# Performance work log

Measured on AMD Instinct MI355X. Metric: run time of the kernel, lower is better.

## Reference

```python
import jax, jax.numpy as jnp
import numpy as np

B, L = 2, 2048
D_MODEL, D_INNER, D_STATE, DT_RANK, D_CONV, DEPTH = 1024, 2048, 16, 64, 4, 2
EPS = 1e-5


def setup_inputs() -> dict:
    key = jax.random.key(0)
    ks = jax.random.split(key, 8)
    rn = lambda k, s, scale=0.02: jax.random.normal(k, s, jnp.float32) * scale
    return {
        "x": jax.random.normal(ks[0], (B, L, D_MODEL), jnp.float32),
        "x_size": L,  # truthiness flag only; unused in the math
        "norm_w": jnp.ones((DEPTH, D_MODEL), jnp.float32),
        "norm_b": jnp.zeros((DEPTH, D_MODEL), jnp.float32),
        "in_proj_w": rn(ks[1], (DEPTH, 2 * D_INNER, D_MODEL)),
        "conv_w": rn(ks[2], (DEPTH, D_INNER, 1, D_CONV), 0.1),
        "conv_b": jnp.zeros((DEPTH, D_INNER), jnp.float32),
        "x_proj_w": rn(ks[3], (DEPTH, DT_RANK + 2 * D_STATE, D_INNER)),
        "dt_proj_w": rn(ks[4], (DEPTH, D_INNER, DT_RANK), 0.1),
        "dt_proj_b": jnp.full((DEPTH, D_INNER), -4.0, jnp.float32),  # softplus -> small dt
        "A_log": jnp.broadcast_to(
            jnp.log(jnp.arange(1, D_STATE + 1, dtype=jnp.float32)), (DEPTH, D_INNER, D_STATE)
        ) + jnp.zeros((DEPTH, D_INNER, D_STATE), jnp.float32),
        "D": jnp.ones((DEPTH, D_INNER), jnp.float32),
        "out_proj_w": rn(ks[5], (DEPTH, D_MODEL, D_INNER)),
    }


def _layernorm(x, w, b):
    mu = x.mean(-1, keepdims=True)
    var = ((x - mu) ** 2).mean(-1, keepdims=True)
    return (x - mu) * jax.lax.rsqrt(var + EPS) * w + b


def _selective_scan(u, dt, A, Bm, Cm, Dp):
    # u, dt: (B, L, di); A: (di, n); Bm, Cm: (B, L, n); Dp: (di,)
    def step(h, inp):
        u_t, dt_t, B_t, C_t = inp  # (B,di), (B,di), (B,n), (B,n)
        dA = jnp.exp(dt_t[..., None] * A)                       # (B, di, n)
        h = dA * h + (dt_t * u_t)[..., None] * B_t[:, None, :]  # (B, di, n)
        y = jnp.einsum('bdn,bn->bd', h, C_t)
        return h, y

    h0 = jnp.zeros((u.shape[0], A.shape[0], A.shape[1]), u.dtype)
    xs = (u.swapaxes(0, 1), dt.swapaxes(0, 1), Bm.swapaxes(0, 1), Cm.swapaxes(0, 1))
    _, ys = jax.lax.scan(step, h0, xs)  # ys: (L, B, di)
    return ys.swapaxes(0, 1) + u * Dp


def _mamba(x, in_proj_w, conv_w, conv_b, x_proj_w, dt_proj_w, dt_proj_b, A_log, Dp, out_proj_w):
    xz = jnp.einsum('bld,ed->ble', x, in_proj_w)  # (B, L, 2*di)
    u, z = jnp.split(xz, 2, axis=-1)
    # causal depthwise conv1d, kernel D_CONV
    uc = jax.lax.conv_general_dilated(
        u.swapaxes(1, 2), conv_w, (1,), [(D_CONV - 1, 0)],
        feature_group_count=D_INNER, dimension_numbers=('NCH', 'OIH', 'NCH'))
    u = jax.nn.silu(uc.swapaxes(1, 2) + conv_b)
    x_dbl = jnp.einsum('bld,ed->ble', u, x_proj_w)
    dt_r, Bm, Cm = jnp.split(x_dbl, [DT_RANK, DT_RANK + D_STATE], axis=-1)
    dt = jax.nn.softplus(jnp.einsum('blr,dr->bld', dt_r, dt_proj_w) + dt_proj_b)
    A = -jnp.exp(A_log)
    y = _selective_scan(u, dt, A, Bm, Cm, Dp)
    y = y * jax.nn.silu(z)
    return jnp.einsum('bld,ed->ble', y, out_proj_w)


def reference(x, x_size, norm_w, norm_b, in_proj_w, conv_w, conv_b, x_proj_w,
              dt_proj_w, dt_proj_b, A_log, D, out_proj_w):
    # BasicLayer passes x_size as `residual` (non-None), so each Block reduces to
    # x <- Mamba(LN(x)); the returned residual is discarded by x = blk(...)[0].
    h = x
    for i in range(DEPTH):
        hn = _layernorm(h, norm_w[i], norm_b[i])
        h = _mamba(hn, in_proj_w[i], conv_w[i], conv_b[i], x_proj_w[i],
                   dt_proj_w[i], dt_proj_b[i], A_log[i], D[i], out_proj_w[i])
    return h
```

## Files before the change

### kernel.cpp

```cpp
#include <hip/hip_runtime.h>
#include <hip/hip_bf16.h>
#include <math.h>

#define BQ 2
#define LQ 2048
#define D_MODEL 1024
#define D_INNER 2048
#define D_STATE 16
#define DT_RANK 64
#define D_CONV 4
#define DEPTH 2
#define NCHUNK 64
#define CHUNK 32
#define XSPLITK 8
#define XKC (D_INNER / XSPLITK)

typedef __attribute__((ext_vector_type(8))) short short8v;
typedef __attribute__((ext_vector_type(4))) float f32x4;

__device__ __forceinline__ short f2bf(float f) {
    union { float f; unsigned u; } v; v.f = f;
    unsigned r = v.u + 0x7fffu + ((v.u >> 16) & 1u);
    return (short)(r >> 16);
}

__device__ __forceinline__ float bf2f(unsigned short s) {
    union { unsigned u; float f; } v; v.u = ((unsigned)s) << 16;
    return v.f;
}

__device__ __forceinline__ void async16(void* lds, const void* gp) {
    __builtin_amdgcn_global_load_lds(
        (const __attribute__((address_space(1))) void*)gp,
        (__attribute__((address_space(3))) void*)lds, 16, 0, 0);
}

__global__ __launch_bounds__(256) void layernorm_kernel(
    const float* __restrict__ x, const float* __restrict__ w,
    const float* __restrict__ b, short* __restrict__ out)
{
    __shared__ float red[8];
    int row = blockIdx.x;
    const float* xr = x + (size_t)row * D_MODEL;
    float v[4];
    float s = 0.f, sq = 0.f;
#pragma unroll
    for (int i = 0; i < 4; ++i) {
        v[i] = xr[threadIdx.x + i * 256];
        s += v[i];
        sq += v[i] * v[i];
    }
#pragma unroll
    for (int off = 32; off; off >>= 1) {
        s += __shfl_down(s, off, 64);
        sq += __shfl_down(sq, off, 64);
    }
    int wid = threadIdx.x >> 6, lane = threadIdx.x & 63;
    if (!lane) { red[wid] = s; red[4 + wid] = sq; }
    __syncthreads();
    s = red[0] + red[1] + red[2] + red[3];
    sq = red[4] + red[5] + red[6] + red[7];
    float mu = s * (1.f / D_MODEL);
    float var = sq * (1.f / D_MODEL) - mu * mu;
    float rstd = rsqrtf(var + 1e-5f);
#pragma unroll
    for (int i = 0; i < 4; ++i) {
        int c = threadIdx.x + i * 256;
        out[(size_t)row * D_MODEL + c] = f2bf((v[i] - mu) * rstd * w[c] + b[c]);
    }
}

__global__ __launch_bounds__(512) void gemm256_bf16_kernel(
    const short* __restrict__ A, const short* __restrict__ W,
    short* __restrict__ C, int M, int N, int K)
{
    __shared__ __align__(16) short lds[65536];
    const int tid = threadIdx.x;
    const int lane = tid & 63;
    const int w = tid >> 6;
    const int wr = w >> 2, wc = w & 3;

    int nbx = N >> 8;
    int nwg = (M >> 8) * nbx;
    int q = nwg >> 3;
    int wg = ((int)blockIdx.x & 7) * q + ((int)blockIdx.x >> 3);
    int bx = wg % nbx, by = wg / nbx;
    int bm = by << 8, bn = bx << 8;

    const int fr = lane & 15;
    const int kl = lane >> 4;
    const int srow = lane >> 3;
    const int schunk = (lane & 7) ^ (srow & 7);

    f32x4 acc[8][4] = {};
    short8v af[4][2], bfA[2][2], bfB[2][2];

    auto STAGE = [&](int isA, int buf, int half, int kt) {
        const short* gp = isA ? A : W;
        int tile0 = isA ? bm : bn;
        int base = (isA ? 0 : 32768) + (buf * 2 + half) * 8192;
        int ko = kt << 6;
#pragma unroll
        for (int s = 0; s < 2; ++s) {
            int row = half * 128 + s * 64 + w * 8 + srow;
            const short* src = gp + (size_t)(tile0 + row) * K + ko + schunk * 8;
            async16(&lds[base + s * 4096 + w * 512], src);
        }
    };

    auto LOAD_A = [&](int buf, int mh) {
        int abase = (buf * 2 + mh) * 8192;
#pragma unroll
        for (int i = 0; i < 4; ++i) {
            int rl = wr * 64 + i * 16 + fr;
            int rsw = rl & 7;
#pragma unroll
            for (int ks = 0; ks < 2; ++ks)
                af[i][ks] = *(const short8v*)&lds[abase + rl * 64 + (((ks * 4 + kl) ^ rsw) * 8)];
        }
    };
    auto LOAD_B = [&](int buf, int nh, short8v (&bf)[2][2]) {
        int bbase = 32768 + (buf * 2 + nh) * 8192;
#pragma unroll
        for (int j = 0; j < 2; ++j) {
            int rl = wc * 32 + j * 16 + fr;
            int rsw = rl & 7;
#pragma unroll
            for (int ks = 0; ks < 2; ++ks)
                bf[j][ks] = *(const short8v*)&lds[bbase + rl * 64 + (((ks * 4 + kl) ^ rsw) * 8)];
        }
    };
    auto MFMA_Q = [&](int mh, int nh, short8v (&bf)[2][2]) {
        __builtin_amdgcn_s_setprio(1);
#pragma unroll
        for (int i = 0; i < 4; ++i)
#pragma unroll
            for (int j = 0; j < 2; ++j)
#pragma unroll
                for (int ks = 0; ks < 2; ++ks)
                    acc[mh * 4 + i][nh * 2 + j] = __builtin_amdgcn_mfma_f32_16x16x32_bf16(
                        af[i][ks], bf[j][ks], acc[mh * 4 + i][nh * 2 + j], 0, 0, 0);
        __builtin_amdgcn_s_setprio(0);
    };

#define GBAR  __builtin_amdgcn_s_barrier(); __builtin_amdgcn_sched_barrier(0);
#define LGKM  asm volatile("s_waitcnt lgkmcnt(0)" ::: "memory"); __builtin_amdgcn_sched_barrier(0);

    STAGE(1, 0, 0, 0); STAGE(0, 0, 0, 0);
    STAGE(1, 0, 1, 0); STAGE(0, 0, 1, 0);
    STAGE(1, 1, 0, 1); STAGE(0, 1, 0, 1);

    int T = K >> 7;
    for (int t = 0; t < T; ++t) {
        int last = (t == T - 1);
        asm volatile("s_waitcnt vmcnt(4)" ::: "memory");
        STAGE(1, 1, 1, 2 * t + 1);
        GBAR;
        LOAD_A(0, 0); LOAD_B(0, 0, bfA);
        LGKM; MFMA_Q(0, 0, bfA);
        GBAR;
        STAGE(0, 1, 1, 2 * t + 1);
        GBAR;
        LOAD_B(0, 1, bfB);
        LGKM; MFMA_Q(0, 1, bfB);
        GBAR;
        if (!last) STAGE(1, 0, 0, 2 * t + 2);
        GBAR;
        LOAD_A(0, 1);
        LGKM; MFMA_Q(1, 1, bfB);
        GBAR;
        if (!last) STAGE(0, 0, 0, 2 * t + 2);
        GBAR;
        MFMA_Q(1, 0, bfA);
        GBAR;
        if (last) { asm volatile("s_waitcnt vmcnt(0)" ::: "memory"); }
        else      { asm volatile("s_waitcnt vmcnt(4)" ::: "memory"); }
        if (!last) STAGE(1, 0, 1, 2 * t + 2);
        GBAR;
        LOAD_A(1, 0); LOAD_B(1, 0, bfA);
        LGKM; MFMA_Q(0, 0, bfA);
        GBAR;
        if (!last) STAGE(0, 0, 1, 2 * t + 2);
        GBAR;
        LOAD_B(1, 1, bfB);
        LGKM; MFMA_Q(0, 1, bfB);
        GBAR;
        if (!last) STAGE(1, 1, 0, 2 * t + 3);
        GBAR;
        LOAD_A(1, 1);
        LGKM; MFMA_Q(1, 1, bfB);
        GBAR;
        if (!last) STAGE(0, 1, 0, 2 * t + 3);
        GBAR;
        MFMA_Q(1, 0, bfA);
        GBAR;
    }
#undef GBAR
#undef LGKM

    int cr = (lane >> 4) * 4, cc = lane & 15;
#pragma unroll
    for (int i8 = 0; i8 < 8; ++i8) {
        int mh = i8 >> 2, ii = i8 & 3;
        int row0 = bm + mh * 128 + wr * 64 + ii * 16 + cr;
#pragma unroll
        for (int p = 0; p < 4; ++p) {
            short* Cp = C + (size_t)(row0 + p) * N + bn;
#pragma unroll
            for (int j4 = 0; j4 < 4; ++j4) {
                int nh = j4 >> 1, jj = j4 & 1;
                Cp[nh * 128 + wc * 32 + jj * 16 + cc] = f2bf(acc[i8][j4][p]);
            }
        }
    }
}

__global__ __launch_bounds__(256) void gemm_bf16_kernel(
    const short* __restrict__ A, const short* __restrict__ W,
    void* __restrict__ Cv, int M, int N, int K,
    const float* __restrict__ bias, int epilogue)
{
    __shared__ __align__(16) short As[2][128 * 64];
    __shared__ __align__(16) short Bs[2][128 * 64];
    int tid = threadIdx.x;
    int lane = tid & 63, wv = tid >> 6;
    int nbx = N >> 7;
    int nwg = (M >> 7) * nbx;
    int q = nwg >> 3;
    int wg = ((int)blockIdx.x & 7) * q + ((int)blockIdx.x >> 3);
    int bx = wg % nbx, by = wg / nbx;
    int bm = by * 128, bn = bx * 128;
    int wr = wv >> 1, wc = wv & 1;

    const int fr = lane & 15;
    const int kl = lane >> 4;
    const int srow = lane >> 3;
    const int schunk = (lane & 7) ^ (srow & 7);

    f32x4 acc[4][4] = {};

    const short* Ab = A + (size_t)bm * K;
    const short* Bb = W + (size_t)bn * K;

    auto STAGE = [&](int buf, int kt) {
        int ko = kt << 6;
#pragma unroll
        for (int s = 0; s < 4; ++s) {
            int row = s * 32 + wv * 8 + srow;
            async16(&As[buf][s * 2048 + wv * 512], Ab + (size_t)row * K + ko + schunk * 8);
            async16(&Bs[buf][s * 2048 + wv * 512], Bb + (size_t)row * K + ko + schunk * 8);
        }
    };

    int NT = K >> 6;
    STAGE(0, 0);
    if (NT > 1) STAGE(1, 1);

    for (int t = 0; t < NT; ++t) {
        if (t + 1 < NT) { asm volatile("s_waitcnt vmcnt(8)" ::: "memory"); }
        else            { asm volatile("s_waitcnt vmcnt(0)" ::: "memory"); }
        __builtin_amdgcn_s_barrier();
        __builtin_amdgcn_sched_barrier(0);
        int buf = t & 1;
        short8v af[4][2], bf[4][2];
#pragma unroll
        for (int i = 0; i < 4; ++i) {
            int rl = wr * 64 + i * 16 + fr;
            int rsw = rl & 7;
#pragma unroll
            for (int ks = 0; ks < 2; ++ks)
                af[i][ks] = *(const short8v*)&As[buf][rl * 64 + (((ks * 4 + kl) ^ rsw) * 8)];
        }
#pragma unroll
        for (int j = 0; j < 4; ++j) {
            int rl = wc * 64 + j * 16 + fr;
            int rsw = rl & 7;
#pragma unroll
            for (int ks = 0; ks < 2; ++ks)
                bf[j][ks] = *(const short8v*)&Bs[buf][rl * 64 + (((ks * 4 + kl) ^ rsw) * 8)];
        }
        asm volatile("s_waitcnt lgkmcnt(0)" ::: "memory");
        __builtin_amdgcn_sched_barrier(0);
        __builtin_amdgcn_s_setprio(1);
#pragma unroll
        for (int i = 0; i < 4; ++i)
#pragma unroll
            for (int j = 0; j < 4; ++j)
#pragma unroll
                for (int ks = 0; ks < 2; ++ks)
                    acc[i][j] = __builtin_amdgcn_mfma_f32_16x16x32_bf16(
                        af[i][ks], bf[j][ks], acc[i][j], 0, 0, 0);
        __builtin_amdgcn_s_setprio(0);
        __builtin_amdgcn_s_barrier();
        __builtin_amdgcn_sched_barrier(0);
        if (t + 2 < NT) STAGE(buf, t + 2);
    }

    int cr = (lane >> 4) * 4, cc = lane & 15;
#pragma unroll
    for (int i = 0; i < 4; ++i)
#pragma unroll
        for (int p = 0; p < 4; ++p) {
            int row = bm + wr * 64 + i * 16 + cr + p;
#pragma unroll
            for (int j = 0; j < 4; ++j) {
                int col = bn + wc * 64 + cc + j * 16;
                float v = acc[i][j][p];
                if (epilogue == 2)
                    ((short*)Cv)[(size_t)row * N + col] = f2bf(v);
                else
                    ((float*)Cv)[(size_t)row * N + col] = v;
            }
        }
}

__global__ __launch_bounds__(256) void dtproj_kernel(
    const short* __restrict__ A, const short* __restrict__ W,
    const float* __restrict__ bias, short* __restrict__ Out)
{
    int lane = threadIdx.x & 63, w = threadIdx.x >> 6;
    int m0 = blockIdx.y * 64 + w * 16;
    int bn = blockIdx.x * 128;
    int fr = lane & 15, fk = (lane >> 4) * 8;
    const short* Ap = A + (size_t)(m0 + fr) * DT_RANK + fk;
    short8v a0 = *(const short8v*)(Ap);
    short8v a1 = *(const short8v*)(Ap + 32);
    f32x4 acc[8] = {};
#pragma unroll
    for (int j = 0; j < 8; ++j) {
        const short* Wp = W + (size_t)(bn + j * 16 + fr) * DT_RANK + fk;
        short8v b0 = *(const short8v*)(Wp);
        short8v b1 = *(const short8v*)(Wp + 32);
        acc[j] = __builtin_amdgcn_mfma_f32_16x16x32_bf16(a0, b0, acc[j], 0, 0, 0);
        acc[j] = __builtin_amdgcn_mfma_f32_16x16x32_bf16(a1, b1, acc[j], 0, 0, 0);
    }
    int cr = (lane >> 4) * 4, cc = lane & 15;
#pragma unroll
    for (int j = 0; j < 8; ++j) {
        int col = bn + j * 16 + cc;
        float bv = bias[col];
#pragma unroll
        for (int p = 0; p < 4; ++p) {
            float v = acc[j][p] + bv;
            v = (v > 20.f) ? v : __logf(1.f + __expf(v));
            Out[(size_t)(m0 + cr + p) * D_INNER + col] = f2bf(v);
        }
    }
}

__global__ __launch_bounds__(256) void xproj_kernel(
    const short* __restrict__ A, const short* __restrict__ W,
    float* __restrict__ Xpart)
{
    int lane = threadIdx.x & 63, wv = threadIdx.x >> 6;
    int sk = blockIdx.x;
    int m0 = blockIdx.y * 64 + wv * 16;
    int fr = lane & 15, fk = (lane >> 4) * 8;
    const short* Ap = A + (size_t)(m0 + fr) * D_INNER + sk * XKC + fk;
    const short* Wp = W + (size_t)fr * D_INNER + sk * XKC + fk;
    f32x4 acc[6] = {};
    for (int k = 0; k < XKC; k += 32) {
        short8v af = *(const short8v*)(Ap + k);
#pragma unroll
        for (int j = 0; j < 6; ++j) {
            short8v bf = *(const short8v*)(Wp + (size_t)j * 16 * D_INNER + k);
            acc[j] = __builtin_amdgcn_mfma_f32_16x16x32_bf16(af, bf, acc[j], 0, 0, 0);
        }
    }
    int cr = (lane >> 4) * 4, cc = lane & 15;
    float* Op = Xpart + ((size_t)sk * (BQ * LQ) + m0 + cr) * 96 + cc;
#pragma unroll
    for (int j = 0; j < 6; ++j)
#pragma unroll
        for (int p = 0; p < 4; ++p)
            Op[(size_t)p * 96 + j * 16] = acc[j][p];
}

__global__ __launch_bounds__(256) void xreduce_kernel(
    const float* __restrict__ Xpart, float* __restrict__ xdbl,
    short* __restrict__ dtr)
{
    size_t i = (size_t)blockIdx.x * 256 + threadIdx.x;
    float s = 0.f;
#pragma unroll
    for (int sk = 0; sk < XSPLITK; ++sk)
        s += Xpart[(size_t)sk * ((size_t)BQ * LQ * 96) + i];
    xdbl[i] = s;
    int col = (int)(i % 96);
    if (col < DT_RANK)
        dtr[(i / 96) * DT_RANK + col] = f2bf(s);
}

__global__ __launch_bounds__(256) void conv_silu_kernel(
    const unsigned short* __restrict__ uz, short* __restrict__ outb,
    const float* __restrict__ w, const float* __restrict__ bias)
{
    int idx = blockIdx.x * 256 + threadIdx.x;
    int c = idx & (D_INNER - 1);
    int bl = idx / D_INNER;
    int l = bl & (LQ - 1);
    int b = bl / LQ;
    float acc = bias[c];
#pragma unroll
    for (int k = 0; k < D_CONV; ++k) {
        int ls = l - (D_CONV - 1) + k;
        if (ls >= 0)
            acc += bf2f(uz[((size_t)b * LQ + ls) * (2 * D_INNER) + c]) * w[c * D_CONV + k];
    }
    float val = acc / (1.f + __expf(-acc));
    outb[idx] = f2bf(val);
}

__global__ __launch_bounds__(256) void scan_phase1_kernel(
    const unsigned short* __restrict__ u, const unsigned short* __restrict__ dt,
    const float* __restrict__ xdbl, const float* __restrict__ A_log,
    float* __restrict__ Pbuf, float* __restrict__ Fbuf)
{
    __shared__ float S[CHUNK][D_STATE];
    int t = threadIdx.x;
    int d = blockIdx.x * 256 + t;
    int c = blockIdx.y;
    int b = blockIdx.z;
    int l0 = c * CHUNK;
    {
        int row = t >> 3, cc2 = (t & 7) * 2;
        const float* src = xdbl + ((size_t)(b * LQ + l0 + row)) * 96 + DT_RANK + cc2;
        *(float2*)&S[row][cc2] = *(const float2*)src;
    }
    float A[D_STATE], h[D_STATE];
    {
        const float4* ap = (const float4*)(A_log + (size_t)d * D_STATE);
#pragma unroll
        for (int g = 0; g < 4; ++g) {
            float4 a = ap[g];
            A[g*4+0] = -__expf(a.x); A[g*4+1] = -__expf(a.y);
            A[g*4+2] = -__expf(a.z); A[g*4+3] = -__expf(a.w);
        }
    }
#pragma unroll
    for (int n = 0; n < D_STATE; ++n) h[n] = 0.f;
    float dtsum = 0.f;
    const unsigned short* up  = u  + ((size_t)b * LQ + l0) * D_INNER + d;
    const unsigned short* dtp = dt + ((size_t)b * LQ + l0) * D_INNER + d;
    __syncthreads();

    for (int lb = 0; lb < CHUNK; lb += 8) {
        float uvv[8], dtvv[8];
#pragma unroll
        for (int i = 0; i < 8; ++i) {
            uvv[i]  = bf2f(up [(size_t)(lb + i) * D_INNER]);
            dtvv[i] = bf2f(dtp[(size_t)(lb + i) * D_INNER]);
        }
#pragma unroll
        for (int i = 0; i < 8; ++i) {
            int l = lb + i;
            float dtv = dtvv[i];
            float du = dtv * uvv[i];
            dtsum += dtv;
#pragma unroll
            for (int n4 = 0; n4 < D_STATE; n4 += 4) {
                float4 Bv = *(const float4*)&S[l][n4];
                float bb[4] = {Bv.x, Bv.y, Bv.z, Bv.w};
#pragma unroll
                for (int k = 0; k < 4; ++k) {
                    int n = n4 + k;
                    float dA = __expf(dtv * A[n]);
                    h[n] = dA * h[n] + du * bb[k];
                }
            }
        }
    }
    size_t base = ((size_t)(b * NCHUNK + c) * D_STATE) * D_INNER + d;
#pragma unroll
    for (int n = 0; n < D_STATE; ++n) {
        Pbuf[base + (size_t)n * D_INNER] = __expf(A[n] * dtsum);
        Fbuf[base + (size_t)n * D_INNER] = h[n];
    }
}

__global__ __launch_bounds__(256) void scan_phase2_kernel(
    const float* __restrict__ Pbuf, float* __restrict__ Fbuf)
{
    int d = blockIdx.x * 256 + threadIdx.x;
    int n = blockIdx.y;
    int b = blockIdx.z;
    float hinit = 0.f;
    for (int c = 0; c < NCHUNK; ++c) {
        size_t idx = ((size_t)(b * NCHUNK + c) * D_STATE + n) * D_INNER + d;
        float P = Pbuf[idx];
        float F = Fbuf[idx];
        Fbuf[idx] = hinit;
        hinit = P * hinit + F;
    }
}

__global__ __launch_bounds__(256) void scan_phase3_kernel(
    const unsigned short* __restrict__ u, const unsigned short* __restrict__ dt,
    const float* __restrict__ xdbl, const float* __restrict__ A_log,
    const float* __restrict__ Dp, const float* __restrict__ Hinit,
    const unsigned short* __restrict__ uz, short* __restrict__ yout)
{
    __shared__ float S[CHUNK][32];
    int t = threadIdx.x;
    int d = blockIdx.x * 256 + t;
    int c = blockIdx.y;
    int b = blockIdx.z;
    int l0 = c * CHUNK;
    {
        int row = t >> 3, cg = (t & 7) * 4;
        const float* src = xdbl + ((size_t)(b * LQ + l0 + row)) * 96 + DT_RANK + cg;
        *(float4*)&S[row][cg ^ ((row & 7) << 2)] = *(const float4*)src;
    }
    float A[D_STATE], h[D_STATE];
    {
        const float4* ap = (const float4*)(A_log + (size_t)d * D_STATE);
#pragma unroll
        for (int g = 0; g < 4; ++g) {
            float4 a = ap[g];
            A[g*4+0] = -__expf(a.x); A[g*4+1] = -__expf(a.y);
            A[g*4+2] = -__expf(a.z); A[g*4+3] = -__expf(a.w);
        }
    }
    size_t base = ((size_t)(b * NCHUNK + c) * D_STATE) * D_INNER + d;
#pragma unroll
    for (int n = 0; n < D_STATE; ++n)
        h[n] = Hinit[base + (size_t)n * D_INNER];
    float Dd = Dp[d];
    const unsigned short* up  = u  + ((size_t)b * LQ + l0) * D_INNER + d;
    const unsigned short* dtp = dt + ((size_t)b * LQ + l0) * D_INNER + d;
    const unsigned short* zp = uz + ((size_t)b * LQ + l0) * (2 * D_INNER) + D_INNER + d;
    short* yp = yout + ((size_t)b * LQ + l0) * D_INNER + d;
    __syncthreads();

    for (int lb = 0; lb < CHUNK; lb += 8) {
        float uvv[8], dtvv[8], zvv[8];
#pragma unroll
        for (int i = 0; i < 8; ++i) {
            uvv[i]  = bf2f(up [(size_t)(lb + i) * D_INNER]);
            dtvv[i] = bf2f(dtp[(size_t)(lb + i) * D_INNER]);
            zvv[i]  = bf2f(zp [(size_t)(lb + i) * (2 * D_INNER)]);
        }
#pragma unroll
        for (int i = 0; i < 8; ++i) {
            int l = lb + i;
            float dtv = dtvv[i];
            float du = dtv * uvv[i];
            float acc = 0.f;
            int sw = (l & 7) << 2;
#pragma unroll
            for (int n4 = 0; n4 < D_STATE; n4 += 4) {
                float4 Bv = *(const float4*)&S[l][n4 ^ sw];
                float4 Cv = *(const float4*)&S[l][(16 + n4) ^ sw];
                float bb[4] = {Bv.x, Bv.y, Bv.z, Bv.w};
                float cc[4] = {Cv.x, Cv.y, Cv.z, Cv.w};
#pragma unroll
                for (int k = 0; k < 4; ++k) {
                    int n = n4 + k;
                    float dA = __expf(dtv * A[n]);
                    h[n] = dA * h[n] + du * bb[k];
                    acc += h[n] * cc[k];
                }
            }
            float y = acc + uvv[i] * Dd;
            float zv = zvv[i];
            float g = zv / (1.f + __expf(-zv));
            yp[(size_t)l * D_INNER] = f2bf(y * g);
        }
    }
}

__global__ __launch_bounds__(256) void convert_bf16_kernel(
    const float* __restrict__ in, short* __restrict__ out)
{
    int i = (blockIdx.x * 256 + threadIdx.x) * 4;
    float4 v = *(const float4*)(in + i);
    short4 o = make_short4(f2bf(v.x), f2bf(v.y), f2bf(v.z), f2bf(v.w));
    *(short4*)(out + i) = o;
}

extern "C" void kernel_launch(void* const* d_in, const int* in_sizes, int n_in,
                              void* d_out, int out_size, void* d_ws, size_t ws_size,
                              hipStream_t stream)
{
    const float* x        = (const float*)d_in[0];
    const float* norm_w   = (const float*)d_in[2];
    const float* norm_b   = (const float*)d_in[3];
    const float* in_proj  = (const float*)d_in[4];
    const float* conv_w   = (const float*)d_in[5];
    const float* conv_b   = (const float*)d_in[6];
    const float* x_proj   = (const float*)d_in[7];
    const float* dt_proj  = (const float*)d_in[8];
    const float* dt_projb = (const float*)d_in[9];
    const float* A_log    = (const float*)d_in[10];
    const float* Dp       = (const float*)d_in[11];
    const float* out_proj = (const float*)d_in[12];
    float* out = (float*)d_out;
    float* ws  = (float*)d_ws;

    const size_t BL   = (size_t)BQ * LQ;
    const size_t BLDM = BL * D_MODEL;
    const size_t BLDI = BL * D_INNER;
    const int IN_W  = 2 * D_INNER * D_MODEL;
    const int OUT_W = D_MODEL * D_INNER;
    const int XP_W  = 96 * D_INNER;
    const int DT_W  = D_INNER * DT_RANK;

    size_t o = 0;
    float* Pbuf  = ws + o; o += BLDM;
    short* uzb   = (short*)(ws + o); o += BL * 2 * D_INNER / 2;
    short* dtb   = (short*)(ws + o); o += BLDI;
    float* xdbl  = ws + o; o += BL * 96;
    float* h1    = ws + o; o += BLDM;
    float* Fbuf  = ws + o; o += BLDM;
    short* ucx   = (short*)(ws + o); o += BLDI / 2;
    short* dtr   = (short*)(ws + o); o += BL * DT_RANK / 2;
    short* wbuf  = (short*)(ws + o);
    o += (size_t)(IN_W + OUT_W + XP_W + DT_W + 1) / 2;

    short* hnb = (short*)Pbuf;
    float* Xpart = h1;

    for (int layer = 0; layer < DEPTH; ++layer) {
        const float* src = (layer == 0) ? x : h1;
        float* dst = (layer == DEPTH - 1) ? out : h1;

        layernorm_kernel<<<(int)BL, 256, 0, stream>>>(
            src, norm_w + (size_t)layer * D_MODEL, norm_b + (size_t)layer * D_MODEL, hnb);

        convert_bf16_kernel<<<IN_W / 1024, 256, 0, stream>>>(
            in_proj + (size_t)layer * IN_W, wbuf);
        convert_bf16_kernel<<<OUT_W / 1024, 256, 0, stream>>>(
            out_proj + (size_t)layer * OUT_W, wbuf + IN_W);
        convert_bf16_kernel<<<XP_W / 1024, 256, 0, stream>>>(
            x_proj + (size_t)layer * XP_W, wbuf + IN_W + OUT_W);
        convert_bf16_kernel<<<DT_W / 1024, 256, 0, stream>>>(
            dt_proj + (size_t)layer * DT_W, wbuf + IN_W + OUT_W + XP_W);

        gemm256_bf16_kernel<<<(int)(BL / 256) * (2 * D_INNER / 256), 512, 0, stream>>>(
            hnb, wbuf, uzb, (int)BL, 2 * D_INNER, D_MODEL);

        conv_silu_kernel<<<(int)(BLDI / 256), 256, 0, stream>>>(
            (const unsigned short*)uzb, ucx,
            conv_w + (size_t)layer * D_INNER * D_CONV,
            conv_b + (size_t)layer * D_INNER);

        xproj_kernel<<<dim3(XSPLITK, BL / 64), 256, 0, stream>>>(
            ucx, wbuf + IN_W + OUT_W, Xpart);
        xreduce_kernel<<<(int)(BL * 96 / 256), 256, 0, stream>>>(Xpart, xdbl, dtr);

        dtproj_kernel<<<dim3(D_INNER / 128, BL / 64), 256, 0, stream>>>(
            dtr, wbuf + IN_W + OUT_W + XP_W,
            dt_projb + (size_t)layer * D_INNER, dtb);

        const float* Al = A_log + (size_t)layer * D_INNER * D_STATE;
        scan_phase1_kernel<<<dim3(D_INNER / 256, NCHUNK, BQ), 256, 0, stream>>>(
            (const unsigned short*)ucx, (const unsigned short*)dtb, xdbl, Al, Pbuf, Fbuf);
        scan_phase2_kernel<<<dim3(D_INNER / 256, D_STATE, BQ), 256, 0, stream>>>(
            Pbuf, Fbuf);
        scan_phase3_kernel<<<dim3(D_INNER / 256, NCHUNK, BQ), 256, 0, stream>>>(
            (const unsigned short*)ucx, (const unsigned short*)dtb, xdbl, Al,
            Dp + (size_t)layer * D_INNER, Fbuf,
            (const unsigned short*)uzb, (short*)ucx);

        gemm_bf16_kernel<<<(int)(BL / 128) * (D_MODEL / 128), 256, 0, stream>>>(
            ucx, wbuf + IN_W, dst, (int)BL, D_MODEL, D_INNER, nullptr, 0);
    }
}
```

Baseline: 500.1 us.

## Split-K the out_proj GEMM and fuse weight conversion launches

The out_proj GEMM (M=4096, N=1024, K=2048) previously launched only 256 workgroups. It now splits K in two, giving 512 workgroups that write fp32 partials, and a new osum kernel adds the two partials into the destination. The four per-layer weight-conversion launches are merged into one kernel that picks its source and destination by block index. The dtb workspace allocation is halved to match its bf16 size. Split-K adds extra fp32 partial traffic (about 32MB written and read) plus one more launch, in exchange for better CU occupancy on the GEMM.

After: 484.0 us. 3.2% less time.

```diff
diff --git a/kernel.cpp b/kernel.cpp
--- a/kernel.cpp
+++ b/kernel.cpp
@@ -14,6 +14,7 @@
 #define CHUNK 32
 #define XSPLITK 8
 #define XKC (D_INNER / XSPLITK)
+#define OSK 2
 
 typedef __attribute__((ext_vector_type(8))) short short8v;
 typedef __attribute__((ext_vector_type(4))) float f32x4;
@@ -218,7 +219,7 @@
 __global__ __launch_bounds__(256) void gemm_bf16_kernel(
     const short* __restrict__ A, const short* __restrict__ W,
     void* __restrict__ Cv, int M, int N, int K,
-    const float* __restrict__ bias, int epilogue)
+    const float* __restrict__ bias, int epilogue, int nsk)
 {
     __shared__ __align__(16) short As[2][128 * 64];
     __shared__ __align__(16) short Bs[2][128 * 64];
@@ -226,11 +227,16 @@
     int lane = tid & 63, wv = tid >> 6;
     int nbx = N >> 7;
     int nwg = (M >> 7) * nbx;
-    int q = nwg >> 3;
-    int wg = ((int)blockIdx.x & 7) * q + ((int)blockIdx.x >> 3);
+    int ntot = nwg * nsk;
+    int q = ntot >> 3;
+    int wgz = ((int)blockIdx.x & 7) * q + ((int)blockIdx.x >> 3);
+    int sk = wgz / nwg;
+    int wg = wgz % nwg;
     int bx = wg % nbx, by = wg / nbx;
     int bm = by * 128, bn = bx * 128;
     int wr = wv >> 1, wc = wv & 1;
+    int Kl = K / nsk;
+    int koff = sk * Kl;
 
     const int fr = lane & 15;
     const int kl = lane >> 4;
@@ -239,8 +245,8 @@
 
     f32x4 acc[4][4] = {};
 
-    const short* Ab = A + (size_t)bm * K;
-    const short* Bb = W + (size_t)bn * K;
+    const short* Ab = A + (size_t)bm * K + koff;
+    const short* Bb = W + (size_t)bn * K + koff;
 
     auto STAGE = [&](int buf, int kt) {
         int ko = kt << 6;
@@ -252,7 +258,7 @@
         }
     };
 
-    int NT = K >> 6;
+    int NT = Kl >> 6;
     STAGE(0, 0);
     if (NT > 1) STAGE(1, 1);
 
@@ -297,6 +303,7 @@
     }
 
     int cr = (lane >> 4) * 4, cc = lane & 15;
+    size_t skoff = (size_t)sk * M * N;
 #pragma unroll
     for (int i = 0; i < 4; ++i)
 #pragma unroll
@@ -309,9 +316,19 @@
                 if (epilogue == 2)
                     ((short*)Cv)[(size_t)row * N + col] = f2bf(v);
                 else
-                    ((float*)Cv)[(size_t)row * N + col] = v;
+                    ((float*)Cv)[skoff + (size_t)row * N + col] = v;
             }
         }
+}
+
+__global__ __launch_bounds__(256) void osum_kernel(
+    const float* __restrict__ P, float* __restrict__ out)
+{
+    size_t i = ((size_t)blockIdx.x * 256 + threadIdx.x) * 4;
+    float4 a = *(const float4*)(P + i);
+    float4 b = *(const float4*)(P + (size_t)BQ * LQ * D_MODEL + i);
+    a.x += b.x; a.y += b.y; a.z += b.z; a.w += b.w;
+    *(float4*)(out + i) = a;
 }
 
 __global__ __launch_bounds__(256) void dtproj_kernel(
@@ -569,13 +586,24 @@
     }
 }
 
-__global__ __launch_bounds__(256) void convert_bf16_kernel(
-    const float* __restrict__ in, short* __restrict__ out)
-{
-    int i = (blockIdx.x * 256 + threadIdx.x) * 4;
-    float4 v = *(const float4*)(in + i);
+__global__ __launch_bounds__(256) void convert_all_kernel(
+    const float* __restrict__ w_in, const float* __restrict__ w_out,
+    const float* __restrict__ w_xp, const float* __restrict__ w_dt,
+    short* __restrict__ wbuf)
+{
+    const int IN_B  = (2 * D_INNER * D_MODEL) / 1024;
+    const int OUT_B = (D_MODEL * D_INNER) / 1024;
+    const int XP_B  = (96 * D_INNER) / 1024;
+    int blk = blockIdx.x;
+    const float* src; short* dst;
+    if (blk < IN_B)                 { src = w_in;  dst = wbuf; }
+    else if (blk < IN_B + OUT_B)    { src = w_out; dst = wbuf + 2 * D_INNER * D_MODEL; blk -= IN_B; }
+    else if (blk < IN_B + OUT_B + XP_B) { src = w_xp; dst = wbuf + 2 * D_INNER * D_MODEL + D_MODEL * D_INNER; blk -= IN_B + OUT_B; }
+    else { src = w_dt; dst = wbuf + 2 * D_INNER * D_MODEL + D_MODEL * D_INNER + 96 * D_INNER; blk -= IN_B + OUT_B + XP_B; }
+    int i = blk * 1024 + threadIdx.x * 4;
+    float4 v = *(const float4*)(src + i);
     short4 o = make_short4(f2bf(v.x), f2bf(v.y), f2bf(v.z), f2bf(v.w));
-    *(short4*)(out + i) = o;
+    *(short4*)(dst + i) = o;
 }
 
 extern "C" void kernel_launch(void* const* d_in, const int* in_sizes, int n_in,
@@ -604,16 +632,18 @@
     const int OUT_W = D_MODEL * D_INNER;
     const int XP_W  = 96 * D_INNER;
     const int DT_W  = D_INNER * DT_RANK;
+    const int CV_BLOCKS = (IN_W + OUT_W + XP_W + DT_W) / 1024;
 
     size_t o = 0;
     float* Pbuf  = ws + o; o += BLDM;
     short* uzb   = (short*)(ws + o); o += BL * 2 * D_INNER / 2;
-    short* dtb   = (short*)(ws + o); o += BLDI;
+    short* dtb   = (short*)(ws + o); o += BLDI / 2;
     float* xdbl  = ws + o; o += BL * 96;
     float* h1    = ws + o; o += BLDM;
     float* Fbuf  = ws + o; o += BLDM;
     short* ucx   = (short*)(ws + o); o += BLDI / 2;
     short* dtr   = (short*)(ws + o); o += BL * DT_RANK / 2;
+    float* Opart = ws + o; o += (size_t)OSK * BLDM;
     short* wbuf  = (short*)(ws + o);
     o += (size_t)(IN_W + OUT_W + XP_W + DT_W + 1) / 2;
 
@@ -627,14 +657,9 @@
         layernorm_kernel<<<(int)BL, 256, 0, stream>>>(
             src, norm_w + (size_t)layer * D_MODEL, norm_b + (size_t)layer * D_MODEL, hnb);
 
-        convert_bf16_kernel<<<IN_W / 1024, 256, 0, stream>>>(
-            in_proj + (size_t)layer * IN_W, wbuf);
-        convert_bf16_kernel<<<OUT_W / 1024, 256, 0, stream>>>(
-            out_proj + (size_t)layer * OUT_W, wbuf + IN_W);
-        convert_bf16_kernel<<<XP_W / 1024, 256, 0, stream>>>(
-            x_proj + (size_t)layer * XP_W, wbuf + IN_W + OUT_W);
-        convert_bf16_kernel<<<DT_W / 1024, 256, 0, stream>>>(
-            dt_proj + (size_t)layer * DT_W, wbuf + IN_W + OUT_W + XP_W);
+        convert_all_kernel<<<CV_BLOCKS, 256, 0, stream>>>(
+            in_proj + (size_t)layer * IN_W, out_proj + (size_t)layer * OUT_W,
+            x_proj + (size_t)layer * XP_W, dt_proj + (size_t)layer * DT_W, wbuf);
 
         gemm256_bf16_kernel<<<(int)(BL / 256) * (2 * D_INNER / 256), 512, 0, stream>>>(
             hnb, wbuf, uzb, (int)BL, 2 * D_INNER, D_MODEL);
@@ -662,7 +687,8 @@
             Dp + (size_t)layer * D_INNER, Fbuf,
             (const unsigned short*)uzb, (short*)ucx);
 
-        gemm_bf16_kernel<<<(int)(BL / 128) * (D_MODEL / 128), 256, 0, stream>>>(
-            ucx, wbuf + IN_W, dst, (int)BL, D_MODEL, D_INNER, nullptr, 0);
-    }
-}
+        gemm_bf16_kernel<<<(int)(BL / 128) * (D_MODEL / 128) * OSK, 256, 0, stream>>>(
+            ucx, wbuf + IN_W, Opart, (int)BL, D_MODEL, D_INNER, nullptr, 0, OSK);
+        osum_kernel<<<(int)(BLDM / 1024), 256, 0, stream>>>(Opart, dst);
+    }
+}
```
